# Kernel optimization log

Measured on AMD Instinct MI355X. Metric: run time of the kernel, lower is better.

The kernel has to match this reference:

```python
import jax, jax.numpy as jnp
import numpy as np

B, C, H, W = 16, 512, 32, 32
COND_C, L_COND = 768, 77
N_GROUPS, N_HEADS = 8, 8
HEAD = C // N_HEADS
EPS = 1e-5


def setup_inputs() -> dict:
    key = jax.random.key(0)
    ks = jax.random.split(key, 6)
    s = lambda fan_in: 1.0 / np.sqrt(fan_in)
    return {
        "x_0": jax.random.normal(ks[0], (B, C, H, W), jnp.float32),
        "cond": jax.random.normal(ks[1], (B, L_COND, COND_C), jnp.float32),
        "gn_gamma": jnp.ones((C,), jnp.float32),
        "gn_beta": jnp.zeros((C,), jnp.float32),
        "qkv_w": jax.random.normal(ks[2], (3 * C, C), jnp.float32) * s(C),
        "qkv_b": jnp.zeros((3 * C,), jnp.float32),
        "cond_kv_w": jax.random.normal(ks[3], (2 * C, COND_C), jnp.float32) * s(COND_C),
        "cond_kv_b": jnp.zeros((2 * C,), jnp.float32),
        "out_w": jax.random.normal(ks[4], (C, C), jnp.float32) * s(C),
        "out_b": jnp.zeros((C,), jnp.float32),
    }


def reference(x_0, cond, gn_gamma, gn_beta, qkv_w, qkv_b, cond_kv_w, cond_kv_b, out_w, out_b):
    b, c, h, w = x_0.shape
    L = h * w
    # --- GroupNorm over (C/G, H, W) per group, per-channel affine ---
    xg = x_0.reshape(b, N_GROUPS, c // N_GROUPS, h * w)
    mu = xg.mean(axis=(2, 3), keepdims=True)
    var = xg.var(axis=(2, 3), keepdims=True)
    xn = ((xg - mu) * jax.lax.rsqrt(var + EPS)).reshape(b, c, h, w)
    xn = xn * gn_gamma[None, :, None, None] + gn_beta[None, :, None, None]
    # --- to tokens [B, L, C] ---
    x = xn.transpose(0, 2, 3, 1).reshape(b, L, c)
    # --- QKV ---
    qkv = x @ qkv_w.T + qkv_b  # [B, L, 3C]
    q, k, v = jnp.split(qkv, 3, axis=-1)
    q = q.reshape(b, L, N_HEADS, HEAD)
    k = k.reshape(b, L, N_HEADS, HEAD)
    v = v.reshape(b, L, N_HEADS, HEAD)
    # --- conditional K/V ---
    kv_c = cond @ cond_kv_w.T + cond_kv_b  # [B, Lc, 2C]
    k_c, v_c = jnp.split(kv_c, 2, axis=-1)
    Lc = cond.shape[1]
    k_c = k_c.reshape(b, Lc, N_HEADS, HEAD)
    v_c = v_c.reshape(b, Lc, N_HEADS, HEAD)
    K = jnp.concatenate([k, k_c], axis=1)  # [B, L+Lc, H, D]
    V = jnp.concatenate([v, v_c], axis=1)
    # --- attention (full score matrix, as in the original) ---
    scale = HEAD ** -0.5
    scores = jnp.einsum("bqhd,bkhd->bhqk", q, K) * scale
    att = jax.nn.softmax(scores, axis=-1)
    out = jnp.einsum("bhqk,bkhd->bqhd", att, V).reshape(b, L, c)
    out = out @ out_w.T + out_b
    # --- back to image + residual ---
    out = out.reshape(b, h, w, c).transpose(0, 3, 1, 2)
    return out + x_0
```

## Files before the change

### kernel.cpp

```cpp
#include <hip/hip_runtime.h>

typedef short bf16x8 __attribute__((ext_vector_type(8)));
typedef float f32x4 __attribute__((ext_vector_type(4)));
typedef float f32x16 __attribute__((ext_vector_type(16)));
typedef unsigned int u32x4 __attribute__((ext_vector_type(4)));

#define KVP 1152

__device__ __forceinline__ unsigned short f2b(float f) {
    unsigned int u = __float_as_uint(f);
    u += 0x7FFFu + ((u >> 16) & 1u);
    return (unsigned short)(u >> 16);
}

__device__ __forceinline__ f32x4 mfma16(bf16x8 a, bf16x8 b, f32x4 c) {
    return __builtin_amdgcn_mfma_f32_16x16x32_bf16(a, b, c, 0, 0, 0);
}
__device__ __forceinline__ f32x16 mfma32(bf16x8 a, bf16x8 b, f32x16 c) {
    return __builtin_amdgcn_mfma_f32_32x32x16_bf16(a, b, c, 0, 0, 0);
}
__device__ __forceinline__ float exp2_raw(float x) {
    float r; asm("v_exp_f32 %0, %1" : "=v"(r) : "v"(x)); return r;
}
__device__ __forceinline__ unsigned cvt_pk(float lo, float hi) {
    unsigned r; asm("v_cvt_pk_bf16_f32 %0, %1, %2" : "=v"(r) : "v"(lo), "v"(hi)); return r;
}
__device__ __forceinline__ float f3(float a, float b, float c) { return fmaxf(fmaxf(a, b), c); }

typedef __attribute__((address_space(3))) unsigned int lds_u32_t;
typedef const __attribute__((address_space(1))) unsigned int glb_u32_t;
__device__ __forceinline__ void async_cp16(const void* g, void* l) {
    __builtin_amdgcn_global_load_lds((glb_u32_t*)(unsigned long long)g,
                                     (lds_u32_t*)(unsigned int)(unsigned long long)l,
                                     16, 0, 0);
}

__global__ __launch_bounds__(256) void prep_k(const float* __restrict__ x, float2* __restrict__ part,
                                              const float* __restrict__ a, unsigned short* __restrict__ oa,
                                              const float* __restrict__ b, unsigned short* __restrict__ ob,
                                              const float* __restrict__ c, unsigned short* __restrict__ oc,
                                              const float* __restrict__ d, unsigned short* __restrict__ od) {
    if (blockIdx.x < 512) {
        int blk = blockIdx.x;
        const float4* p = (const float4*)(x + (size_t)blk * 16384);
        float s = 0.f, ss = 0.f;
        for (int i = threadIdx.x; i < 4096; i += 256) {
            float4 v = p[i];
            s  += v.x + v.y + v.z + v.w;
            ss += v.x * v.x + v.y * v.y + v.z * v.z + v.w * v.w;
        }
#pragma unroll
        for (int o = 32; o; o >>= 1) { s += __shfl_down(s, o); ss += __shfl_down(ss, o); }
        __shared__ float red[8];
        int w = threadIdx.x >> 6;
        if ((threadIdx.x & 63) == 0) { red[w] = s; red[4 + w] = ss; }
        __syncthreads();
        if (threadIdx.x == 0) {
            s  = red[0] + red[1] + red[2] + red[3];
            ss = red[4] + red[5] + red[6] + red[7];
            part[blk] = make_float2(s, ss);
        }
        return;
    }
    int i = (blockIdx.x - 512) * 256 + threadIdx.x;
    const float* src; unsigned short* dst; int j;
    if (i < 196608)      { src = a; dst = oa; j = i; }
    else if (i < 393216) { src = b; dst = ob; j = i - 196608; }
    else if (i < 458752) { src = c; dst = oc; j = i - 393216; }
    else if (i < 695296) { src = d; dst = od; j = i - 458752; }
    else return;
    float4 v = ((const float4*)src)[j];
    uint2 u = make_uint2(cvt_pk(v.x, v.y), cvt_pk(v.z, v.w));
    ((uint2*)dst)[j] = u;
}

__global__ __launch_bounds__(256) void gn_apply_k(const float* __restrict__ x, const float2* __restrict__ part,
                                                  const float* __restrict__ gamma, const float* __restrict__ beta,
                                                  unsigned short* __restrict__ xt) {
    int st = blockIdx.x & 15;
    int ct = (blockIdx.x >> 4) & 7;
    int b  = blockIdx.x >> 7;
    int bg = b * 8 + ct;
    float2 p0 = part[4 * bg], p1 = part[4 * bg + 1], p2 = part[4 * bg + 2], p3 = part[4 * bg + 3];
    float s = (p0.x + p1.x) + (p2.x + p3.x);
    float ss = (p0.y + p1.y) + (p2.y + p3.y);
    float mean = s * (1.f / 65536.f);
    float var  = ss * (1.f / 65536.f) - mean * mean;
    float rsig = rsqrtf(var + 1e-5f);
    __shared__ unsigned short tile[64][65];
    int tid = threadIdx.x;
#pragma unroll
    for (int it = 0; it < 4; ++it) {
        int idx = it * 256 + tid;
        int ci = idx >> 4, j4 = idx & 15;
        int c = ct * 64 + ci;
        float4 v = *(const float4*)(x + ((size_t)b * 512 + c) * 1024 + st * 64 + j4 * 4);
        float gs = gamma[c] * rsig;
        float bo = beta[c] - mean * gs;
        tile[j4 * 4 + 0][ci] = f2b(v.x * gs + bo);
        tile[j4 * 4 + 1][ci] = f2b(v.y * gs + bo);
        tile[j4 * 4 + 2][ci] = f2b(v.z * gs + bo);
        tile[j4 * 4 + 3][ci] = f2b(v.w * gs + bo);
    }
    __syncthreads();
#pragma unroll
    for (int it = 0; it < 4; ++it) {
        int idx = it * 256 + tid;
        int si = idx >> 4, q = idx & 15;
        uint2 u;
        u.x = (unsigned)tile[si][q * 4 + 0] | ((unsigned)tile[si][q * 4 + 1] << 16);
        u.y = (unsigned)tile[si][q * 4 + 2] | ((unsigned)tile[si][q * 4 + 3] << 16);
        *(uint2*)(xt + ((size_t)b * 1024 + st * 64 + si) * 512 + ct * 64 + q * 4) = u;
    }
}

template <int EPI>
__global__ __launch_bounds__(512) void gemm256_k(const unsigned short* __restrict__ A,
                                                 const unsigned short* __restrict__ Bw,
                                                 const float* __restrict__ bias,
                                                 int K,
                                                 unsigned short* __restrict__ Qo,
                                                 unsigned short* __restrict__ Ko,
                                                 unsigned short* __restrict__ Vo,
                                                 const float* __restrict__ x0,
                                                 float* __restrict__ outp) {
    __shared__ __align__(16) unsigned short As[3][256 * 64];
    __shared__ __align__(16) unsigned short Bs[3][128 * 64];
    const int m0 = blockIdx.x * 256, n0 = blockIdx.y * 128;
    const bool swp = (EPI == 0) && (blockIdx.y < 8);
    const int tid = threadIdx.x, lane = tid & 63, w = tid >> 6;
    const int wr = w >> 1, wc = w & 1;
    const int lc = lane & 15, lg = lane >> 4;

    const int r8 = lane >> 3;
    const int sSw = ((lane & 7) ^ (r8 & 7)) * 8;
    const unsigned short* aS = A + (size_t)(m0 + w * 32 + r8) * K + sSw;
    const unsigned short* bS = Bw + (size_t)(n0 + w * 16 + r8) * K + sSw;

    f32x4 acc[4][4];
#pragma unroll
    for (int m = 0; m < 4; ++m)
#pragma unroll
        for (int n = 0; n < 4; ++n) acc[m][n] = (f32x4){0.f, 0.f, 0.f, 0.f};

    const int nT = K >> 6;

#define STAGE64(tile, buf)                                                             \
    {                                                                                  \
        const int k0_ = (tile) << 6;                                                   \
        async_cp16(aS + k0_,                    &As[buf][(w * 32) * 64]);              \
        async_cp16(aS + k0_ + (size_t)8 * K,    &As[buf][(w * 32 + 8) * 64]);          \
        async_cp16(aS + k0_ + (size_t)16 * K,   &As[buf][(w * 32 + 16) * 64]);         \
        async_cp16(aS + k0_ + (size_t)24 * K,   &As[buf][(w * 32 + 24) * 64]);         \
        async_cp16(bS + k0_,                    &Bs[buf][(w * 16) * 64]);              \
        async_cp16(bS + k0_ + (size_t)8 * K,    &Bs[buf][(w * 16 + 8) * 64]);          \
    }

    STAGE64(0, 0);

    int c = 0;
#pragma unroll 1
    for (int t = 0; t < nT; ++t) {
        if (t + 1 < nT) {
            int c1 = c + 1; if (c1 == 3) c1 = 0;
            STAGE64(t + 1, c1);
            asm volatile("s_waitcnt vmcnt(6)" ::: "memory");
        } else {
            asm volatile("s_waitcnt vmcnt(0)" ::: "memory");
        }
        __builtin_amdgcn_s_barrier();

#pragma unroll
        for (int kk = 0; kk < 2; ++kk) {
            bf16x8 af[4], bfr[4];
#pragma unroll
            for (int m = 0; m < 4; ++m) {
                const int row = wr * 64 + m * 16 + lc;
                af[m] = *(const bf16x8*)&As[c][row * 64 + (((kk * 4 + lg) ^ (lc & 7)) * 8)];
            }
#pragma unroll
            for (int n = 0; n < 4; ++n) {
                const int row = wc * 64 + n * 16 + lc;
                bfr[n] = *(const bf16x8*)&Bs[c][row * 64 + (((kk * 4 + lg) ^ (lc & 7)) * 8)];
            }
            __builtin_amdgcn_s_setprio(1);
            if (swp) {
#pragma unroll
                for (int m = 0; m < 4; ++m)
#pragma unroll
                    for (int n = 0; n < 4; ++n)
                        acc[m][n] = mfma16(bfr[n], af[m], acc[m][n]);
            } else {
#pragma unroll
                for (int m = 0; m < 4; ++m)
#pragma unroll
                    for (int n = 0; n < 4; ++n)
                        acc[m][n] = mfma16(af[m], bfr[n], acc[m][n]);
            }
            __builtin_amdgcn_s_setprio(0);
        }

        ++c; if (c == 3) c = 0;
    }
#undef STAGE64

    if (EPI == 0) {
        if (swp) {
            const bool isQ = (n0 < 512);
            const float sc = isQ ? (0.125f * 1.44269504089f) : 1.f;
#pragma unroll
            for (int n = 0; n < 4; ++n) {
                const int c0 = n0 + wc * 64 + n * 16 + lg * 4;
                const float4 b4 = *(const float4*)&bias[c0];
#pragma unroll
                for (int m = 0; m < 4; ++m) {
                    const int tok = m0 + wr * 64 + m * 16 + lc;
                    const int b = tok >> 10, l = tok & 1023;
                    float v0 = (acc[m][n][0] + b4.x) * sc;
                    float v1 = (acc[m][n][1] + b4.y) * sc;
                    float v2 = (acc[m][n][2] + b4.z) * sc;
                    float v3 = (acc[m][n][3] + b4.w) * sc;
                    uint2 u = make_uint2(cvt_pk(v0, v1), cvt_pk(v2, v3));
                    if (isQ) {
                        const int hh = c0 >> 6, d = c0 & 63;
                        *(uint2*)(Qo + ((size_t)(b * 8 + hh) * 1024 + l) * 64 + d) = u;
                    } else {
                        const int hh = (c0 - 512) >> 6, d = c0 & 63;
                        *(uint2*)(Ko + ((size_t)(b * 8 + hh) * KVP + l) * 64 + d) = u;
                    }
                }
            }
        } else {
#pragma unroll
            for (int n = 0; n < 4; ++n) {
                const int col = n0 + wc * 64 + n * 16 + lc;
                const int j = col - 1024;
                const int hh = j >> 6, d = j & 63;
                const float bv = bias[col];
#pragma unroll
                for (int m = 0; m < 4; ++m) {
                    const int t0 = m0 + wr * 64 + m * 16 + lg * 4;
                    const int b = t0 >> 10, l0 = t0 & 1023;
                    uint2 u = make_uint2(cvt_pk(acc[m][n][0] + bv, acc[m][n][1] + bv),
                                         cvt_pk(acc[m][n][2] + bv, acc[m][n][3] + bv));
                    *(uint2*)(Vo + ((size_t)(b * 8 + hh) * 64 + d) * KVP + l0) = u;
                }
            }
        }
    } else {
#pragma unroll
        for (int n = 0; n < 4; ++n) {
            const int col = n0 + wc * 64 + n * 16 + lc;
            const float bv = bias[col];
#pragma unroll
            for (int m = 0; m < 4; ++m) {
                const int t0 = m0 + wr * 64 + m * 16 + lg * 4;
                const size_t a = ((size_t)(t0 >> 10) * 512 + col) * 1024 + (t0 & 1023);
                float4 xv = *(const float4*)(x0 + a);
                float4 o;
                o.x = acc[m][n][0] + bv + xv.x;
                o.y = acc[m][n][1] + bv + xv.y;
                o.z = acc[m][n][2] + bv + xv.z;
                o.w = acc[m][n][3] + bv + xv.w;
                *(float4*)(outp + a) = o;
            }
        }
    }
}

__global__ __launch_bounds__(256) void gemm_nt_k(const unsigned short* __restrict__ A,
                                                 const unsigned short* __restrict__ Bw,
                                                 const float* __restrict__ bias,
                                                 int M, int N, int K,
                                                 unsigned short* __restrict__ Ko,
                                                 unsigned short* __restrict__ Vo) {
    __shared__ unsigned short As[64][40];
    __shared__ unsigned short Bs[64][40];
    const int m0 = blockIdx.x * 64, n0 = blockIdx.y * 64;
    const int tid = threadIdx.x, lane = tid & 63, w = tid >> 6;
    const int lc = lane & 15, lg = lane >> 4;
    const int lrow = tid >> 2, lseg = tid & 3;
    f32x4 acc[4];
#pragma unroll
    for (int i = 0; i < 4; ++i) acc[i] = (f32x4){0.f, 0.f, 0.f, 0.f};

    for (int k0 = 0; k0 < K; k0 += 32) {
        uint4 av = make_uint4(0u, 0u, 0u, 0u);
        if (m0 + lrow < M) av = *(const uint4*)(A + (size_t)(m0 + lrow) * K + k0 + lseg * 8);
        *(uint4*)&As[lrow][lseg * 8] = av;
        uint4 bv = *(const uint4*)(Bw + (size_t)(n0 + lrow) * K + k0 + lseg * 8);
        *(uint4*)&Bs[lrow][lseg * 8] = bv;
        __syncthreads();
        bf16x8 af = *(const bf16x8*)&As[w * 16 + lc][lg * 8];
#pragma unroll
        for (int ct = 0; ct < 4; ++ct) {
            bf16x8 bfr = *(const bf16x8*)&Bs[ct * 16 + lc][lg * 8];
            acc[ct] = mfma16(af, bfr, acc[ct]);
        }
        __syncthreads();
    }

    const int rbase = m0 + w * 16 + lg * 4;
#pragma unroll
    for (int ct = 0; ct < 4; ++ct) {
        int col = n0 + ct * 16 + lc;
        float bv = bias[col];
#pragma unroll
        for (int r = 0; r < 4; ++r) {
            int token = rbase + r;
            if (token >= M) continue;
            float val = acc[ct][r] + bv;
            int b = token / 77, l = token - b * 77;
            if (col < 512) {
                int hh = col >> 6, d = col & 63;
                Ko[((size_t)(b * 8 + hh) * KVP + 1024 + l) * 64 + d] = f2b(val);
            } else {
                int j = col - 512, hh = j >> 6, d = j & 63;
                Vo[((size_t)(b * 8 + hh) * 64 + d) * KVP + 1024 + l] = f2b(val);
            }
        }
    }
}

__global__ __launch_bounds__(512) void attn2_k(const unsigned short* __restrict__ Q,
                                               const unsigned short* __restrict__ Kb,
                                               const unsigned short* __restrict__ Vt,
                                               unsigned short* __restrict__ atok) {
    __shared__ __align__(16) unsigned short lds[18432];

    const int bid = blockIdx.x;
    const int bh = bid & 127;
    const int qt = bid >> 7;
    const int w  = threadIdx.x >> 6;
    const int lane = threadIdx.x & 63;
    const int ql = lane & 31, hi = lane >> 5;
    const int q0 = qt * 256 + w * 32;

    bf16x8 qf[4];
    const unsigned short* Qp = Q + ((size_t)bh * 1024 + q0 + ql) * 64 + hi * 8;
#pragma unroll
    for (int ks = 0; ks < 4; ++ks) qf[ks] = *(const bf16x8*)(Qp + ks * 16);

    const unsigned short* Kg = Kb + (size_t)bh * KVP * 64;
    const unsigned short* Vg = Vt + (size_t)bh * 64 * KVP;

    const int srow = lane >> 3;
    const int sc   = (((lane & 7) ^ (lane >> 3)) << 3);

    f32x16 o0, o1;
#pragma unroll
    for (int i = 0; i < 16; ++i) { o0[i] = 0.f; o1[i] = 0.f; }
    float mreg = -1e30f, lsum = 0.f;

    {
        uint4 kr = *(const uint4*)(Kg + (size_t)(8 * w + srow) * 64 + sc);
        uint4 vr = *(const uint4*)(Vg + (size_t)(8 * w + srow) * KVP + sc);
        *(uint4*)&lds[w * 512 + lane * 8] = kr;
        *(uint4*)&lds[4096 + w * 512 + lane * 8] = vr;
    }
    __syncthreads();

    int cur = 0;
    for (int it = 0; it < 18; ++it) {
        const int kv0 = it * 64;
        const bool pre = (it < 17);
        uint4 kn, vn;
        if (pre) {
            kn = *(const uint4*)(Kg + (size_t)(kv0 + 64 + 8 * w + srow) * 64 + sc);
            vn = *(const uint4*)(Vg + (size_t)(8 * w + srow) * KVP + kv0 + 64 + sc);
        }
        const int kb = cur * 8192, vb = cur * 8192 + 4096;

        f32x16 s0, s1;
#pragma unroll
        for (int i = 0; i < 16; ++i) { s0[i] = 0.f; s1[i] = 0.f; }
        __builtin_amdgcn_s_setprio(1);
#pragma unroll
        for (int ks = 0; ks < 4; ++ks) {
            const int sl = ((ks * 2 + hi) ^ (ql & 7)) << 3;
            bf16x8 kf0 = *(const bf16x8*)&lds[kb + ql * 64 + sl];
            bf16x8 kf1 = *(const bf16x8*)&lds[kb + (32 + ql) * 64 + sl];
            s0 = mfma32(kf0, qf[ks], s0);
            s1 = mfma32(kf1, qf[ks], s1);
        }
        __builtin_amdgcn_s_setprio(0);
        if (kv0 == 1088) {
#pragma unroll
            for (int r = 0; r < 16; ++r) {
                int kva = 1088 + (r & 3) + 8 * (r >> 2) + 4 * hi;
                if (kva >= 1101) s0[r] = -1e30f;
                if (kva + 32 >= 1101) s1[r] = -1e30f;
            }
        }

        float t[16];
#pragma unroll
        for (int i = 0; i < 16; ++i) t[i] = fmaxf(s0[i], s1[i]);
        float a0m = f3(t[0], t[1], t[2]),  a1m = f3(t[3], t[4], t[5]);
        float a2m = f3(t[6], t[7], t[8]),  a3m = f3(t[9], t[10], t[11]);
        float a4m = f3(t[12], t[13], t[14]);
        float pm  = fmaxf(f3(a0m, a1m, a2m), f3(a3m, a4m, t[15]));
        float pmax = fmaxf(pm, __shfl_xor(pm, 32));

        if (__any(pmax > mreg + 8.f)) {
            float mn = fmaxf(mreg, pmax);
            float al = exp2_raw(mreg - mn);
            mreg = mn;
            lsum *= al;
#pragma unroll
            for (int i = 0; i < 16; ++i) { o0[i] *= al; o1[i] *= al; }
        }

        unsigned pk0[8], pk1[8];
        float sA = 0.f, sB = 0.f, sC = 0.f, sD = 0.f;
#pragma unroll
        for (int i = 0; i < 8; ++i) {
            float a0 = exp2_raw(s0[2 * i] - mreg), a1 = exp2_raw(s0[2 * i + 1] - mreg);
            float b0 = exp2_raw(s1[2 * i] - mreg), b1 = exp2_raw(s1[2 * i + 1] - mreg);
            pk0[i] = cvt_pk(a0, a1);
            pk1[i] = cvt_pk(b0, b1);
            sA += a0; sB += a1; sC += b0; sD += b1;
        }
        float ls = (sA + sB) + (sC + sD);
        ls += __shfl_xor(ls, 32);
        lsum += ls;

#pragma unroll
        for (int t2 = 0; t2 < 2; ++t2) {
            const unsigned* pk = t2 ? pk1 : pk0;
#pragma unroll
            for (int v = 0; v < 2; ++v) {
                unsigned a0 = pk[4 * v], a1 = pk[4 * v + 1], a2 = pk[4 * v + 2], a3 = pk[4 * v + 3];
                unsigned x = __shfl_xor(hi ? a0 : a2, 32);
                unsigned y = __shfl_xor(hi ? a1 : a3, 32);
                u32x4 fw;
                fw.x = hi ? x : a0; fw.y = hi ? y : a1; fw.z = hi ? a2 : x; fw.w = hi ? a3 : y;
                bf16x8 pf = __builtin_bit_cast(bf16x8, fw);
                const int ks2 = 2 * t2 + v;
                const int sl = ((ks2 * 2 + hi) ^ (ql & 7)) << 3;
                bf16x8 vf0 = *(const bf16x8*)&lds[vb + ql * 64 + sl];
                bf16x8 vf1 = *(const bf16x8*)&lds[vb + (32 + ql) * 64 + sl];
                __builtin_amdgcn_s_setprio(1);
                o0 = mfma32(vf0, pf, o0);
                o1 = mfma32(vf1, pf, o1);
                __builtin_amdgcn_s_setprio(0);
            }
        }

        if (pre) {
            *(uint4*)&lds[(cur ^ 1) * 8192 + w * 512 + lane * 8] = kn;
            *(uint4*)&lds[(cur ^ 1) * 8192 + 4096 + w * 512 + lane * 8] = vn;
        }
        __syncthreads();
        cur ^= 1;
    }

    float rinv = 1.f / lsum;
    unsigned short* sw = &lds[w * 2304];
#pragma unroll
    for (int dt = 0; dt < 2; ++dt) {
#pragma unroll
        for (int rp = 0; rp < 8; ++rp) {
            float e0 = (dt ? o1[2 * rp] : o0[2 * rp]) * rinv;
            float e1 = (dt ? o1[2 * rp + 1] : o0[2 * rp + 1]) * rinv;
            int d = dt * 32 + ((2 * rp) & 3) + 8 * ((2 * rp) >> 2) + 4 * hi;
            *(unsigned*)&sw[ql * 72 + d] = cvt_pk(e0, e1);
        }
    }
    __syncthreads();
    {
        int i = threadIdx.x >> 1, hf = threadIdx.x & 1;
        const unsigned short* src = &lds[(i >> 5) * 2304 + (i & 31) * 72 + hf * 32];
        u32x4 r0 = *(const u32x4*)(src);
        u32x4 r1 = *(const u32x4*)(src + 8);
        u32x4 r2 = *(const u32x4*)(src + 16);
        u32x4 r3 = *(const u32x4*)(src + 24);
        int b = bh >> 3, h = bh & 7;
        unsigned short* gd = atok + ((size_t)b * 1024 + qt * 256 + i) * 512 + h * 64 + hf * 32;
        *(u32x4*)(gd) = r0;
        *(u32x4*)(gd + 8) = r1;
        *(u32x4*)(gd + 16) = r2;
        *(u32x4*)(gd + 24) = r3;
    }
}

extern "C" void kernel_launch(void* const* d_in, const int* in_sizes, int n_in,
                              void* d_out, int out_size, void* d_ws, size_t ws_size,
                              hipStream_t stream) {
    const float* x0     = (const float*)d_in[0];
    const float* cond   = (const float*)d_in[1];
    const float* gamma  = (const float*)d_in[2];
    const float* beta   = (const float*)d_in[3];
    const float* qkv_w  = (const float*)d_in[4];
    const float* qkv_b  = (const float*)d_in[5];
    const float* ckv_w  = (const float*)d_in[6];
    const float* ckv_b  = (const float*)d_in[7];
    const float* out_w  = (const float*)d_in[8];
    const float* out_b  = (const float*)d_in[9];
    float* outp = (float*)d_out;

    char* p = (char*)d_ws;
    float2* part = (float2*)p;           p += 4096;
    unsigned short* xt    = (unsigned short*)p; p += (size_t)16384 * 512 * 2;
    unsigned short* wqkv  = (unsigned short*)p; p += (size_t)1536 * 512 * 2;
    unsigned short* wckv  = (unsigned short*)p; p += (size_t)1024 * 768 * 2;
    unsigned short* wout  = (unsigned short*)p; p += (size_t)512 * 512 * 2;
    unsigned short* condb = (unsigned short*)p; p += (size_t)1232 * 768 * 2;
    unsigned short* Qb    = (unsigned short*)p; p += (size_t)16 * 8 * 1024 * 64 * 2;
    unsigned short* Kb    = (unsigned short*)p; p += (size_t)16 * 8 * KVP * 64 * 2;
    unsigned short* Vtb   = (unsigned short*)p; p += (size_t)16 * 8 * KVP * 64 * 2;
    unsigned short* atok  = (unsigned short*)p; p += (size_t)16384 * 512 * 2;

    prep_k<<<512 + 2716, 256, 0, stream>>>(x0, part, qkv_w, wqkv, ckv_w, wckv, out_w, wout, cond, condb);
    gn_apply_k<<<2048, 256, 0, stream>>>(x0, part, gamma, beta, xt);

    gemm256_k<0><<<dim3(64, 12), 512, 0, stream>>>(xt, wqkv, qkv_b, 512,
                                                   Qb, Kb, Vtb, nullptr, nullptr);
    gemm_nt_k<<<dim3(20, 16), 256, 0, stream>>>(condb, wckv, ckv_b, 1232, 1024, 768, Kb, Vtb);
    attn2_k<<<512, 512, 0, stream>>>(Qb, Kb, Vtb, atok);
    gemm256_k<2><<<dim3(64, 4), 512, 0, stream>>>(atok, wout, out_b, 512,
                                                  nullptr, nullptr, nullptr, x0, outp);
}
```

Measured before the change: 167.0 us.

## Halve GEMM block to four waves each computing a 128x64 tile

```diff
diff --git a/kernel.cpp b/kernel.cpp
--- a/kernel.cpp
+++ b/kernel.cpp
@@ -115,7 +115,7 @@
 }
 
 template <int EPI>
-__global__ __launch_bounds__(512) void gemm256_k(const unsigned short* __restrict__ A,
+__global__ __launch_bounds__(256) void gemm256_k(const unsigned short* __restrict__ A,
                                                  const unsigned short* __restrict__ Bw,
                                                  const float* __restrict__ bias,
                                                  int K,
@@ -129,17 +129,17 @@
     const int m0 = blockIdx.x * 256, n0 = blockIdx.y * 128;
     const bool swp = (EPI == 0) && (blockIdx.y < 8);
     const int tid = threadIdx.x, lane = tid & 63, w = tid >> 6;
-    const int wr = w >> 1, wc = w & 1;
+    const int wM = w >> 1, wN = w & 1;
     const int lc = lane & 15, lg = lane >> 4;
 
     const int r8 = lane >> 3;
     const int sSw = ((lane & 7) ^ (r8 & 7)) * 8;
-    const unsigned short* aS = A + (size_t)(m0 + w * 32 + r8) * K + sSw;
-    const unsigned short* bS = Bw + (size_t)(n0 + w * 16 + r8) * K + sSw;
-
-    f32x4 acc[4][4];
-#pragma unroll
-    for (int m = 0; m < 4; ++m)
+    const unsigned short* aS = A + (size_t)(m0 + w * 64 + r8) * K + sSw;
+    const unsigned short* bS = Bw + (size_t)(n0 + w * 32 + r8) * K + sSw;
+
+    f32x4 acc[8][4];
+#pragma unroll
+    for (int m = 0; m < 8; ++m)
 #pragma unroll
         for (int n = 0; n < 4; ++n) acc[m][n] = (f32x4){0.f, 0.f, 0.f, 0.f};
 
@@ -148,12 +148,18 @@
 #define STAGE64(tile, buf)                                                             \
     {                                                                                  \
         const int k0_ = (tile) << 6;                                                   \
-        async_cp16(aS + k0_,                    &As[buf][(w * 32) * 64]);              \
-        async_cp16(aS + k0_ + (size_t)8 * K,    &As[buf][(w * 32 + 8) * 64]);          \
-        async_cp16(aS + k0_ + (size_t)16 * K,   &As[buf][(w * 32 + 16) * 64]);         \
-        async_cp16(aS + k0_ + (size_t)24 * K,   &As[buf][(w * 32 + 24) * 64]);         \
-        async_cp16(bS + k0_,                    &Bs[buf][(w * 16) * 64]);              \
-        async_cp16(bS + k0_ + (size_t)8 * K,    &Bs[buf][(w * 16 + 8) * 64]);          \
+        async_cp16(aS + k0_,                  &As[buf][(w * 64 +  0) * 64]);           \
+        async_cp16(aS + k0_ + (size_t) 8 * K, &As[buf][(w * 64 +  8) * 64]);           \
+        async_cp16(aS + k0_ + (size_t)16 * K, &As[buf][(w * 64 + 16) * 64]);           \
+        async_cp16(aS + k0_ + (size_t)24 * K, &As[buf][(w * 64 + 24) * 64]);           \
+        async_cp16(aS + k0_ + (size_t)32 * K, &As[buf][(w * 64 + 32) * 64]);           \
+        async_cp16(aS + k0_ + (size_t)40 * K, &As[buf][(w * 64 + 40) * 64]);           \
+        async_cp16(aS + k0_ + (size_t)48 * K, &As[buf][(w * 64 + 48) * 64]);           \
+        async_cp16(aS + k0_ + (size_t)56 * K, &As[buf][(w * 64 + 56) * 64]);           \
+        async_cp16(bS + k0_,                  &Bs[buf][(w * 32 +  0) * 64]);           \
+        async_cp16(bS + k0_ + (size_t) 8 * K, &Bs[buf][(w * 32 +  8) * 64]);           \
+        async_cp16(bS + k0_ + (size_t)16 * K, &Bs[buf][(w * 32 + 16) * 64]);           \
+        async_cp16(bS + k0_ + (size_t)24 * K, &Bs[buf][(w * 32 + 24) * 64]);           \
     }
 
     STAGE64(0, 0);
@@ -164,7 +170,7 @@
         if (t + 1 < nT) {
             int c1 = c + 1; if (c1 == 3) c1 = 0;
             STAGE64(t + 1, c1);
-            asm volatile("s_waitcnt vmcnt(6)" ::: "memory");
+            asm volatile("s_waitcnt vmcnt(12)" ::: "memory");
         } else {
             asm volatile("s_waitcnt vmcnt(0)" ::: "memory");
         }
@@ -172,30 +178,27 @@
 
 #pragma unroll
         for (int kk = 0; kk < 2; ++kk) {
-            bf16x8 af[4], bfr[4];
-#pragma unroll
-            for (int m = 0; m < 4; ++m) {
-                const int row = wr * 64 + m * 16 + lc;
-                af[m] = *(const bf16x8*)&As[c][row * 64 + (((kk * 4 + lg) ^ (lc & 7)) * 8)];
-            }
+            const int slotk = kk * 4;
+            bf16x8 bfr[4];
 #pragma unroll
             for (int n = 0; n < 4; ++n) {
-                const int row = wc * 64 + n * 16 + lc;
-                bfr[n] = *(const bf16x8*)&Bs[c][row * 64 + (((kk * 4 + lg) ^ (lc & 7)) * 8)];
+                const int row = wN * 64 + n * 16 + lc;
+                bfr[n] = *(const bf16x8*)&Bs[c][row * 64 + (((slotk + lg) ^ (lc & 7)) * 8)];
             }
             __builtin_amdgcn_s_setprio(1);
-            if (swp) {
-#pragma unroll
-                for (int m = 0; m < 4; ++m)
+#pragma unroll
+            for (int m = 0; m < 8; ++m) {
+                const int row = wM * 128 + m * 16 + lc;
+                bf16x8 af = *(const bf16x8*)&As[c][row * 64 + (((slotk + lg) ^ (lc & 7)) * 8)];
+                if (swp) {
 #pragma unroll
                     for (int n = 0; n < 4; ++n)
-                        acc[m][n] = mfma16(bfr[n], af[m], acc[m][n]);
-            } else {
-#pragma unroll
-                for (int m = 0; m < 4; ++m)
+                        acc[m][n] = mfma16(bfr[n], af, acc[m][n]);
+                } else {
 #pragma unroll
                     for (int n = 0; n < 4; ++n)
-                        acc[m][n] = mfma16(af[m], bfr[n], acc[m][n]);
+                        acc[m][n] = mfma16(af, bfr[n], acc[m][n]);
+                }
             }
             __builtin_amdgcn_s_setprio(0);
         }
@@ -210,11 +213,11 @@
             const float sc = isQ ? (0.125f * 1.44269504089f) : 1.f;
 #pragma unroll
             for (int n = 0; n < 4; ++n) {
-                const int c0 = n0 + wc * 64 + n * 16 + lg * 4;
+                const int c0 = n0 + wN * 64 + n * 16 + lg * 4;
                 const float4 b4 = *(const float4*)&bias[c0];
 #pragma unroll
-                for (int m = 0; m < 4; ++m) {
-                    const int tok = m0 + wr * 64 + m * 16 + lc;
+                for (int m = 0; m < 8; ++m) {
+                    const int tok = m0 + wM * 128 + m * 16 + lc;
                     const int b = tok >> 10, l = tok & 1023;
                     float v0 = (acc[m][n][0] + b4.x) * sc;
                     float v1 = (acc[m][n][1] + b4.y) * sc;
@@ -233,13 +236,13 @@
         } else {
 #pragma unroll
             for (int n = 0; n < 4; ++n) {
-                const int col = n0 + wc * 64 + n * 16 + lc;
+                const int col = n0 + wN * 64 + n * 16 + lc;
                 const int j = col - 1024;
                 const int hh = j >> 6, d = j & 63;
                 const float bv = bias[col];
 #pragma unroll
-                for (int m = 0; m < 4; ++m) {
-                    const int t0 = m0 + wr * 64 + m * 16 + lg * 4;
+                for (int m = 0; m < 8; ++m) {
+                    const int t0 = m0 + wM * 128 + m * 16 + lg * 4;
                     const int b = t0 >> 10, l0 = t0 & 1023;
                     uint2 u = make_uint2(cvt_pk(acc[m][n][0] + bv, acc[m][n][1] + bv),
                                          cvt_pk(acc[m][n][2] + bv, acc[m][n][3] + bv));
@@ -250,11 +253,11 @@
     } else {
 #pragma unroll
         for (int n = 0; n < 4; ++n) {
-            const int col = n0 + wc * 64 + n * 16 + lc;
+            const int col = n0 + wN * 64 + n * 16 + lc;
             const float bv = bias[col];
 #pragma unroll
-            for (int m = 0; m < 4; ++m) {
-                const int t0 = m0 + wr * 64 + m * 16 + lg * 4;
+            for (int m = 0; m < 8; ++m) {
+                const int t0 = m0 + wM * 128 + m * 16 + lg * 4;
                 const size_t a = ((size_t)(t0 >> 10) * 512 + col) * 1024 + (t0 & 1023);
                 float4 xv = *(const float4*)(x0 + a);
                 float4 o;
@@ -514,10 +517,10 @@
     prep_k<<<512 + 2716, 256, 0, stream>>>(x0, part, qkv_w, wqkv, ckv_w, wckv, out_w, wout, cond, condb);
     gn_apply_k<<<2048, 256, 0, stream>>>(x0, part, gamma, beta, xt);
 
-    gemm256_k<0><<<dim3(64, 12), 512, 0, stream>>>(xt, wqkv, qkv_b, 512,
+    gemm256_k<0><<<dim3(64, 12), 256, 0, stream>>>(xt, wqkv, qkv_b, 512,
                                                    Qb, Kb, Vtb, nullptr, nullptr);
     gemm_nt_k<<<dim3(20, 16), 256, 0, stream>>>(condb, wckv, ckv_b, 1232, 1024, 768, Kb, Vtb);
     attn2_k<<<512, 512, 0, stream>>>(Qb, Kb, Vtb, atok);
-    gemm256_k<2><<<dim3(64, 4), 512, 0, stream>>>(atok, wout, out_b, 512,
+    gemm256_k<2><<<dim3(64, 4), 256, 0, stream>>>(atok, wout, out_b, 512,
                                                   nullptr, nullptr, nullptr, x0, outp);
 }
```

Measured after the change: 189.2 us. 1.13x slower.

## Software-pipeline QK^T of next tile with softmax/PV of previous tile

Applied to the files above, without the earlier changes.

```diff
diff --git a/kernel.cpp b/kernel.cpp
--- a/kernel.cpp
+++ b/kernel.cpp
@@ -326,7 +326,7 @@
                                                const unsigned short* __restrict__ Kb,
                                                const unsigned short* __restrict__ Vt,
                                                unsigned short* __restrict__ atok) {
-    __shared__ __align__(16) unsigned short lds[18432];
+    __shared__ __align__(16) unsigned short lds[24576];
 
     const int bid = blockIdx.x;
     const int bh = bid & 127;
@@ -351,55 +351,16 @@
 #pragma unroll
     for (int i = 0; i < 16; ++i) { o0[i] = 0.f; o1[i] = 0.f; }
     float mreg = -1e30f, lsum = 0.f;
-
-    {
-        uint4 kr = *(const uint4*)(Kg + (size_t)(8 * w + srow) * 64 + sc);
-        uint4 vr = *(const uint4*)(Vg + (size_t)(8 * w + srow) * KVP + sc);
-        *(uint4*)&lds[w * 512 + lane * 8] = kr;
-        *(uint4*)&lds[4096 + w * 512 + lane * 8] = vr;
-    }
-    __syncthreads();
-
-    int cur = 0;
-    for (int it = 0; it < 18; ++it) {
-        const int kv0 = it * 64;
-        const bool pre = (it < 17);
-        uint4 kn, vn;
-        if (pre) {
-            kn = *(const uint4*)(Kg + (size_t)(kv0 + 64 + 8 * w + srow) * 64 + sc);
-            vn = *(const uint4*)(Vg + (size_t)(8 * w + srow) * KVP + kv0 + 64 + sc);
-        }
-        const int kb = cur * 8192, vb = cur * 8192 + 4096;
-
-        f32x16 s0, s1;
-#pragma unroll
-        for (int i = 0; i < 16; ++i) { s0[i] = 0.f; s1[i] = 0.f; }
-        __builtin_amdgcn_s_setprio(1);
-#pragma unroll
-        for (int ks = 0; ks < 4; ++ks) {
-            const int sl = ((ks * 2 + hi) ^ (ql & 7)) << 3;
-            bf16x8 kf0 = *(const bf16x8*)&lds[kb + ql * 64 + sl];
-            bf16x8 kf1 = *(const bf16x8*)&lds[kb + (32 + ql) * 64 + sl];
-            s0 = mfma32(kf0, qf[ks], s0);
-            s1 = mfma32(kf1, qf[ks], s1);
-        }
-        __builtin_amdgcn_s_setprio(0);
-        if (kv0 == 1088) {
-#pragma unroll
-            for (int r = 0; r < 16; ++r) {
-                int kva = 1088 + (r & 3) + 8 * (r >> 2) + 4 * hi;
-                if (kva >= 1101) s0[r] = -1e30f;
-                if (kva + 32 >= 1101) s1[r] = -1e30f;
-            }
-        }
-
+    f32x16 ps0, ps1;
+
+    auto softmax_pv = [&](const f32x16& a0v, const f32x16& a1v, int vb) {
         float t[16];
 #pragma unroll
-        for (int i = 0; i < 16; ++i) t[i] = fmaxf(s0[i], s1[i]);
-        float a0m = f3(t[0], t[1], t[2]),  a1m = f3(t[3], t[4], t[5]);
-        float a2m = f3(t[6], t[7], t[8]),  a3m = f3(t[9], t[10], t[11]);
-        float a4m = f3(t[12], t[13], t[14]);
-        float pm  = fmaxf(f3(a0m, a1m, a2m), f3(a3m, a4m, t[15]));
+        for (int i = 0; i < 16; ++i) t[i] = fmaxf(a0v[i], a1v[i]);
+        float m0_ = f3(t[0], t[1], t[2]),  m1_ = f3(t[3], t[4], t[5]);
+        float m2_ = f3(t[6], t[7], t[8]),  m3_ = f3(t[9], t[10], t[11]);
+        float m4_ = f3(t[12], t[13], t[14]);
+        float pm  = fmaxf(f3(m0_, m1_, m2_), f3(m3_, m4_, t[15]));
         float pmax = fmaxf(pm, __shfl_xor(pm, 32));
 
         if (__any(pmax > mreg + 8.f)) {
@@ -415,8 +376,8 @@
         float sA = 0.f, sB = 0.f, sC = 0.f, sD = 0.f;
 #pragma unroll
         for (int i = 0; i < 8; ++i) {
-            float a0 = exp2_raw(s0[2 * i] - mreg), a1 = exp2_raw(s0[2 * i + 1] - mreg);
-            float b0 = exp2_raw(s1[2 * i] - mreg), b1 = exp2_raw(s1[2 * i + 1] - mreg);
+            float a0 = exp2_raw(a0v[2 * i] - mreg), a1 = exp2_raw(a0v[2 * i + 1] - mreg);
+            float b0 = exp2_raw(a1v[2 * i] - mreg), b1 = exp2_raw(a1v[2 * i + 1] - mreg);
             pk0[i] = cvt_pk(a0, a1);
             pk1[i] = cvt_pk(b0, b1);
             sA += a0; sB += a1; sC += b0; sD += b1;
@@ -430,11 +391,11 @@
             const unsigned* pk = t2 ? pk1 : pk0;
 #pragma unroll
             for (int v = 0; v < 2; ++v) {
-                unsigned a0 = pk[4 * v], a1 = pk[4 * v + 1], a2 = pk[4 * v + 2], a3 = pk[4 * v + 3];
-                unsigned x = __shfl_xor(hi ? a0 : a2, 32);
-                unsigned y = __shfl_xor(hi ? a1 : a3, 32);
+                unsigned b0 = pk[4 * v], b1 = pk[4 * v + 1], b2 = pk[4 * v + 2], b3 = pk[4 * v + 3];
+                unsigned x = __shfl_xor(hi ? b0 : b2, 32);
+                unsigned y = __shfl_xor(hi ? b1 : b3, 32);
                 u32x4 fw;
-                fw.x = hi ? x : a0; fw.y = hi ? y : a1; fw.z = hi ? a2 : x; fw.w = hi ? a3 : y;
+                fw.x = hi ? x : b0; fw.y = hi ? y : b1; fw.z = hi ? b2 : x; fw.w = hi ? b3 : y;
                 bf16x8 pf = __builtin_bit_cast(bf16x8, fw);
                 const int ks2 = 2 * t2 + v;
                 const int sl = ((ks2 * 2 + hi) ^ (ql & 7)) << 3;
@@ -446,14 +407,59 @@
                 __builtin_amdgcn_s_setprio(0);
             }
         }
-
+    };
+
+    {
+        uint4 kr = *(const uint4*)(Kg + (size_t)(8 * w + srow) * 64 + sc);
+        uint4 vr = *(const uint4*)(Vg + (size_t)(8 * w + srow) * KVP + sc);
+        *(uint4*)&lds[w * 512 + lane * 8] = kr;
+        *(uint4*)&lds[4096 + w * 512 + lane * 8] = vr;
+    }
+    __syncthreads();
+
+#pragma unroll 1
+    for (int it = 0; it < 18; ++it) {
+        const int kv0 = it * 64;
+        const bool pre = (it < 17);
+        uint4 kn, vn;
         if (pre) {
-            *(uint4*)&lds[(cur ^ 1) * 8192 + w * 512 + lane * 8] = kn;
-            *(uint4*)&lds[(cur ^ 1) * 8192 + 4096 + w * 512 + lane * 8] = vn;
+            kn = *(const uint4*)(Kg + (size_t)(kv0 + 64 + 8 * w + srow) * 64 + sc);
+            vn = *(const uint4*)(Vg + (size_t)(8 * w + srow) * KVP + kv0 + 64 + sc);
+        }
+        const int kb = (it % 3) * 8192;
+
+        f32x16 s0, s1;
+#pragma unroll
+        for (int i = 0; i < 16; ++i) { s0[i] = 0.f; s1[i] = 0.f; }
+        __builtin_amdgcn_s_setprio(1);
+#pragma unroll
+        for (int ks = 0; ks < 4; ++ks) {
+            const int sl = ((ks * 2 + hi) ^ (ql & 7)) << 3;
+            bf16x8 kf0 = *(const bf16x8*)&lds[kb + ql * 64 + sl];
+            bf16x8 kf1 = *(const bf16x8*)&lds[kb + (32 + ql) * 64 + sl];
+            s0 = mfma32(kf0, qf[ks], s0);
+            s1 = mfma32(kf1, qf[ks], s1);
+        }
+        __builtin_amdgcn_s_setprio(0);
+
+        if (it > 0) softmax_pv(ps0, ps1, ((it + 2) % 3) * 8192 + 4096);
+        ps0 = s0; ps1 = s1;
+
+        if (pre) {
+            const int nb = ((it + 1) % 3) * 8192;
+            *(uint4*)&lds[nb + w * 512 + lane * 8] = kn;
+            *(uint4*)&lds[nb + 4096 + w * 512 + lane * 8] = vn;
         }
         __syncthreads();
-        cur ^= 1;
-    }
+    }
+
+#pragma unroll
+    for (int r = 0; r < 16; ++r) {
+        int kva = 1088 + (r & 3) + 8 * (r >> 2) + 4 * hi;
+        if (kva >= 1101) ps0[r] = -1e30f;
+        if (kva + 32 >= 1101) ps1[r] = -1e30f;
+    }
+    softmax_pv(ps0, ps1, (17 % 3) * 8192 + 4096);
 
     float rinv = 1.f / lsum;
     unsigned short* sw = &lds[w * 2304];
```

After: 186.5 us. 1.12x slower.
